# Optimization experiments

Measured on AMD Instinct MI355X. Metric: run time of the kernel, lower is better.

Reference implementation:

```python
import jax, jax.numpy as jnp
import numpy as np

V_PATCH = (1, 2, 4, 8, 16, 32)
SN = len(V_PATCH)
BETA = 0.25
RESI = 0.5  # abs(quant_resi)
K_PHI = 4
_ticks = np.linspace(1 / 3 / K_PHI, 1 - 1 / 3 / K_PHI, K_PHI)
PHI_SEL = [int(np.argmin(np.abs(_ticks - si / (SN - 1)))) for si in range(SN)]


def _bicubic_mat(n_in, n_out):
    # torch F.interpolate(mode='bicubic', align_corners=False): a=-0.75, half-pixel, edge clamp.
    a = -0.75
    M = np.zeros((n_out, n_in), np.float32)
    scale = n_in / n_out
    for i in range(n_out):
        x = (i + 0.5) * scale - 0.5
        x0 = int(np.floor(x))
        t = x - x0
        for j in range(-1, 3):
            d = abs(t - j)
            if d < 1.0:
                w = (a + 2) * d ** 3 - (a + 3) * d ** 2 + 1.0
            elif d < 2.0:
                w = a * d ** 3 - 5 * a * d ** 2 + 8 * a * d - 4 * a
            else:
                w = 0.0
            M[i, min(max(x0 + j, 0), n_in - 1)] += w
    return jnp.asarray(M)

_BICUBIC = {pn: _bicubic_mat(pn, V_PATCH[-1]) for pn in V_PATCH[:-1]}


def _phi(h, w, b):
    # Phi: h*(1-r) + Conv2d_3x3(h)*r
    y = jax.lax.conv_general_dilated(h, w, (1, 1), 'SAME',
                                     dimension_numbers=('NCHW', 'OIHW', 'NCHW'))
    y = y + b[None, :, None, None]
    return h * (1.0 - RESI) + y * RESI


def setup_inputs() -> dict:
    key = jax.random.key(0)
    k1, k2, k3, k4 = jax.random.split(key, 4)
    B, C, H = 32, 32, 32
    V = 4096
    return {
        'f_BChw': jax.random.normal(k1, (B, C, H, H), jnp.float32),
        'emb': jax.random.normal(k2, (V, C), jnp.float32) * 0.5,
        'phi_w': jax.random.normal(k3, (K_PHI, C, C, 3, 3), jnp.float32) * 0.05,
        'phi_b': jax.random.normal(k4, (K_PHI, C), jnp.float32) * 0.05,
    }


def reference(f_BChw, emb, phi_w, phi_b):
    f = f_BChw.astype(jnp.float32)
    B, C, H, W = f.shape
    V = emb.shape[0]
    f_ng = jax.lax.stop_gradient(f)
    f_rest = f_ng
    # NOTE: the original uses the NON-inplace `f_hat.add(h_BChw)` so f_hat never accumulates.
    f_hat = jnp.zeros_like(f)
    loss = jnp.float32(0.0)
    hits = jnp.zeros((V,), jnp.float32)
    e_sq = jnp.sum(emb * emb, axis=1)  # [V]
    for si, pn in enumerate(V_PATCH):
        if si != SN - 1:
            # mode='area' downsample; pn divides H so it is exact mean pooling
            r = f_rest.reshape(B, C, pn, H // pn, pn, W // pn).mean(axis=(3, 5))
        else:
            r = f_rest
        z = r.transpose(0, 2, 3, 1).reshape(-1, C)  # [N, C]
        d = jax.lax.stop_gradient(
            jnp.sum(z * z, axis=1, keepdims=True) + e_sq - 2.0 * (z @ emb.T))  # [N, V]
        idx = jnp.argmin(d, axis=1)
        hits = hits + jnp.bincount(idx, length=V).astype(jnp.float32)
        h = emb[idx].reshape(B, pn, pn, C).transpose(0, 3, 1, 2)  # [B, C, pn, pn]
        if si != SN - 1:
            M = _BICUBIC[pn]
            h = jnp.einsum('Hh,bchw,Ww->bcHW', M, h, M)
        h = _phi(h, phi_w[PHI_SEL[si]], phi_b[PHI_SEL[si]])
        # original: f_hat.add(h)  (result discarded -> no-op); f_rest.sub_(h) (in-place)
        f_rest = f_rest - h
        loss = loss + BETA * jnp.mean((jax.lax.stop_gradient(f_hat) - f) ** 2) \
                    + jnp.mean((f_hat - f_ng) ** 2)
    total = jnp.sum(hits)
    p = hits / jnp.maximum(total, 1.0)
    perplexity = jnp.exp(-jnp.sum(p * jnp.log(p + 1e-10)))
    return f_hat, loss, perplexity
```

## Files before the change

kernel.cpp:

```cpp
#include <hip/hip_runtime.h>
#include <math.h>
#include <float.h>

#define BS    32
#define CH    32
#define HH    32
#define VV    4096
#define FELEMS (BS*CH*HH*HH)
#define NROWS_TOTAL 43680

typedef unsigned short ushort_t;
typedef unsigned long long u64_t;
typedef _Float16 half_t;
typedef __attribute__((ext_vector_type(8))) _Float16 half8;
typedef __attribute__((ext_vector_type(4))) float floatx4;

__device__ inline void split2(float x, half_t* h, half_t* l) {
    half_t hh = (half_t)x;
    float r = x - (float)hh;
    *h = hh;
    *l = (half_t)r;
}

__device__ inline unsigned score_key32(float s) {
    unsigned u = __builtin_bit_cast(unsigned, s);
    unsigned m = (u & 0x80000000u) ? ~u : (u | 0x80000000u);
    return ~m;
}

__global__ __launch_bounds__(256) void prep_kernel(const float* __restrict__ f,
                                                   const float* __restrict__ emb,
                                                   const float* __restrict__ phw,
                                                   half_t* __restrict__ whi,
                                                   half_t* __restrict__ wlo,
                                                   half_t* __restrict__ ehi,
                                                   half_t* __restrict__ elo,
                                                   float* __restrict__ nesqh,
                                                   float* __restrict__ hits,
                                                   float* __restrict__ laccp,
                                                   half_t* __restrict__ zhi,
                                                   half_t* __restrict__ zlo,
                                                   u64_t* __restrict__ pk,
                                                   float* __restrict__ zpbase,
                                                   float* __restrict__ dout) {
    int gid = blockIdx.x * 256 + threadIdx.x;
    float4 z4 = {0.f, 0.f, 0.f, 0.f};
    *(float4*)(dout + (size_t)gid * 4) = z4;
    if (gid < VV) hits[gid] = 0.f;
    if (gid < NROWS_TOTAL) pk[gid] = ~0ull;
    for (int j = gid; j < 348160; j += 262144) zpbase[j] = 0.f;
    if (gid < 36864) {
        int k = gid & 7, c = (gid >> 3) & 15, q = (gid >> 7) & 3;
        int t2 = gid >> 9;
        int tau = t2 % 9, m2 = t2 / 9;
        int mt = m2 & 1, phi = m2 >> 1;
        int co = mt * 16 + c, ci = q * 8 + k;
        float w = phw[((size_t)(phi * 32 + co) * 32 + ci) * 9 + tau];
        half_t h, l; split2(w, &h, &l);
        whi[gid] = h; wlo[gid] = l;
    }
    if (gid < VV) {
        int v = gid;
        const float* ep = emb + (size_t)v * CH;
        float s = 0.f;
        half_t h[CH], l[CH];
#pragma unroll
        for (int i = 0; i < CH; i++) {
            float e = ep[i];
            s = fmaf(e, e, s);
            split2(e, &h[i], &l[i]);
        }
        nesqh[v] = -0.5f * s;
#pragma unroll
        for (int q = 0; q < 4; q++) {
            half8 H, L;
#pragma unroll
            for (int k = 0; k < 8; k++) {
                H[k] = h[q * 8 + k];
                L[k] = l[q * 8 + k];
            }
            *(half8*)(ehi + (size_t)v * CH + q * 8) = H;
            *(half8*)(elo + (size_t)v * CH + q * 8) = L;
        }
    }

    const int pair = blockIdx.x;
    const float* base = f + (size_t)pair * 1024;
    float s = 0.f, s2 = 0.f;
    for (int p = threadIdx.x; p < 1024; p += 256) {
        float v = base[p];
        s += v;
        s2 = fmaf(v, v, s2);
    }
    __shared__ float sh[256], sh2[256];
    sh[threadIdx.x] = s;
    sh2[threadIdx.x] = s2;
    __syncthreads();
    for (int o = 128; o > 0; o >>= 1) {
        if (threadIdx.x < o) {
            sh[threadIdx.x]  += sh[threadIdx.x + o];
            sh2[threadIdx.x] += sh2[threadIdx.x + o];
        }
        __syncthreads();
    }
    if (threadIdx.x == 0) {
        split2(sh[0] * (1.0f / 1024.0f), &zhi[pair], &zlo[pair]);
        laccp[pair] = sh2[0];
    }
}

__device__ inline floatx4 score_chain(half8 ah, half8 al,
                                      half8 bh, half8 bl, floatx4 ehv) {
    floatx4 acc;
    acc = __builtin_amdgcn_mfma_f32_16x16x32_f16(ah, bh, ehv, 0, 0, 0);
    acc = __builtin_amdgcn_mfma_f32_16x16x32_f16(ah, bl, acc, 0, 0, 0);
    acc = __builtin_amdgcn_mfma_f32_16x16x32_f16(al, bh, acc, 0, 0, 0);
    return acc;
}

__device__ inline void sel4(const floatx4& acc, int v, float* best, int* bidx) {
#pragma unroll
    for (int r = 0; r < 4; r++) {
        if (acc[r] > best[r]) { best[r] = acc[r]; bidx[r] = v; }
    }
}

template <int RT, int TPW>
__device__ inline void argmin_body(const half8* a1, const half8* a2,
                                   const half_t* __restrict__ ehi,
                                   const half_t* __restrict__ elo,
                                   const float* __restrict__ nesqh,
                                   u64_t* __restrict__ pk, int row0, int t0) {
    const int tid  = threadIdx.x;
    const int wv   = tid >> 6;
    const int lane = tid & 63;
    const int col  = lane & 15;
    const int quad = lane >> 4;

    float best[RT][4];
    int   bidx[RT][4];
#pragma unroll
    for (int rt = 0; rt < RT; rt++)
#pragma unroll
        for (int r = 0; r < 4; r++) { best[rt][r] = -FLT_MAX; bidx[rt][r] = 0; }

    int t = t0 + wv * TPW;
    const int tend = t + TPW;

    size_t eoff = ((size_t)((t << 4) + col) << 5) + (quad << 3);
    half8 nb1 = *(const half8*)(ehi + eoff);
    half8 nb2 = *(const half8*)(elo + eoff);
    float neh = nesqh[(t << 4) + col];

    floatx4 acc[RT];
    int vprev = 0;
    if (RT > 1) acc[RT - 1] = floatx4{-FLT_MAX, -FLT_MAX, -FLT_MAX, -FLT_MAX};

    for (; t < tend; t++) {
        const half8 b1 = nb1, b2 = nb2;
        const floatx4 ehv = {neh, neh, neh, neh};
        const int vcur = (t << 4) + col;
        const int tn = (t + 1 < tend) ? (t + 1) : t;
        const size_t eoff2 = ((size_t)((tn << 4) + col) << 5) + (quad << 3);
        nb1 = *(const half8*)(ehi + eoff2);
        nb2 = *(const half8*)(elo + eoff2);
        neh = nesqh[(tn << 4) + col];

        if (RT == 1) {
            acc[0] = score_chain(a1[0], a2[0], b1, b2, ehv);
            sel4(acc[0], vcur, best[0], bidx[0]);
        } else {
            acc[0] = score_chain(a1[0], a2[0], b1, b2, ehv);
            sel4(acc[RT - 1], vprev, best[RT - 1], bidx[RT - 1]);
#pragma unroll
            for (int rt = 1; rt < RT; rt++) {
                acc[rt] = score_chain(a1[rt], a2[rt], b1, b2, ehv);
                sel4(acc[rt - 1], vcur, best[rt - 1], bidx[rt - 1]);
            }
            vprev = vcur;
        }
    }
    if (RT > 1) sel4(acc[RT - 1], vprev, best[RT - 1], bidx[RT - 1]);

#pragma unroll
    for (int m = 1; m < 16; m <<= 1) {
#pragma unroll
        for (int rt = 0; rt < RT; rt++)
#pragma unroll
            for (int r = 0; r < 4; r++) {
                float s2 = __shfl_xor(best[rt][r], m, 64);
                int   v2 = __shfl_xor(bidx[rt][r], m, 64);
                if (s2 > best[rt][r] ||
                    (s2 == best[rt][r] && v2 < bidx[rt][r])) {
                    best[rt][r] = s2; bidx[rt][r] = v2;
                }
            }
    }

    __shared__ float sbs[4 * RT * 16];
    __shared__ int   sbi[4 * RT * 16];
    if (col == 0) {
#pragma unroll
        for (int rt = 0; rt < RT; rt++)
#pragma unroll
            for (int r = 0; r < 4; r++) {
                int row = rt * 16 + (quad << 2) + r;
                sbs[wv * RT * 16 + row] = best[rt][r];
                sbi[wv * RT * 16 + row] = bidx[rt][r];
            }
    }
    __syncthreads();
    if (tid < RT * 16) {
        float s = sbs[tid];
        int   v = sbi[tid];
        for (int w = 1; w < 4; w++) {
            float s2 = sbs[w * RT * 16 + tid];
            int   v2 = sbi[w * RT * 16 + tid];
            if (s2 > s || (s2 == s && v2 < v)) { s = s2; v = v2; }
        }
        u64_t key = ((u64_t)score_key32(s) << 32) | (unsigned)v;
        atomicMin(pk + row0 + tid, key);
    }
}

template <int RT, int VS>
__global__ __launch_bounds__(256) void argmin_stage(const half_t* __restrict__ zhi,
                                                    const half_t* __restrict__ zlo,
                                                    const half_t* __restrict__ ehi,
                                                    const half_t* __restrict__ elo,
                                                    const float* __restrict__ nesqh,
                                                    u64_t* __restrict__ pk) {
    const int lane = threadIdx.x & 63;
    const int col  = lane & 15;
    const int quad = lane >> 4;
    const int row0 = blockIdx.x * (16 * RT);

    half8 a1[RT], a2[RT];
#pragma unroll
    for (int rt = 0; rt < RT; rt++) {
        size_t off = ((size_t)(row0 + rt * 16 + col) << 5) + (quad << 3);
        a1[rt] = *(const half8*)(zhi + off);
        a2[rt] = *(const half8*)(zlo + off);
    }
    argmin_body<RT, 64 / VS>(a1, a2, ehi, elo, nesqh, pk,
                             row0, (int)blockIdx.y * (256 / VS));
}

template <int RT, int VS, int PN>
__global__ __launch_bounds__(256) void argmin_zp(const float* __restrict__ zp,
                                                 const half_t* __restrict__ ehi,
                                                 const half_t* __restrict__ elo,
                                                 const float* __restrict__ nesqh,
                                                 u64_t* __restrict__ pk) {
    const int lane = threadIdx.x & 63;
    const int col  = lane & 15;
    const int quad = lane >> 4;
    const int row0 = blockIdx.x * (16 * RT);
    constexpr int PSP = 32 / PN;
    const float scale = 1.0f / (float)(PSP * PSP);

    half8 a1[RT], a2[RT];
#pragma unroll
    for (int rt = 0; rt < RT; rt++) {
        const float* p = zp + (size_t)(row0 + rt * 16 + col) * CH + (quad << 3);
        float4 v0 = *(const float4*)p;
        float4 v1 = *(const float4*)(p + 4);
        float s[8] = {v0.x, v0.y, v0.z, v0.w, v1.x, v1.y, v1.z, v1.w};
#pragma unroll
        for (int k = 0; k < 8; k++) {
            half_t h, l;
            split2(s[k] * scale, &h, &l);
            a1[rt][k] = h; a2[rt][k] = l;
        }
    }
    argmin_body<RT, 64 / VS>(a1, a2, ehi, elo, nesqh, pk,
                             row0, (int)blockIdx.y * (256 / VS));
}

__global__ __launch_bounds__(256) void argmin5_fused(const float* __restrict__ frest,
                                                     const half_t* __restrict__ ehi,
                                                     const half_t* __restrict__ elo,
                                                     const float* __restrict__ nesqh,
                                                     u64_t* __restrict__ pk) {
    const int lane = threadIdx.x & 63;
    const int col  = lane & 15;
    const int quad = lane >> 4;
    const int row0 = blockIdx.x * 64;

    half8 a1[4], a2[4];
#pragma unroll
    for (int rt = 0; rt < 4; rt++) {
        int n = row0 + rt * 16 + col;
        int b = n >> 10, i = (n >> 5) & 31, j = n & 31;
        const float* p = frest + ((((size_t)(b * CH + quad * 8)) * HH + i) * HH + j);
#pragma unroll
        for (int k = 0; k < 8; k++) {
            half_t h, l;
            split2(p[(size_t)k * (HH * HH)], &h, &l);
            a1[rt][k] = h; a2[rt][k] = l;
        }
    }
    argmin_body<4, 32>(a1, a2, ehi, elo, nesqh, pk,
                       row0, (int)blockIdx.y * 128);
}

__device__ inline void cubic_w(float xs, int pn, int* ix, float* w) {
    const float a = -0.75f;
    float xf = floorf(xs);
    int x0 = (int)xf;
    float t = xs - xf;
#pragma unroll
    for (int j = -1; j <= 2; j++) {
        float d = fabsf(t - (float)j);
        float ww;
        if (d < 1.0f)      ww = ((a + 2.0f) * d - (a + 3.0f)) * d * d + 1.0f;
        else if (d < 2.0f) ww = ((a * d - 5.0f * a) * d + 8.0f * a) * d - 4.0f * a;
        else               ww = 0.0f;
        int xi = x0 + j;
        xi = xi < 0 ? 0 : (xi > pn - 1 ? pn - 1 : xi);
        ix[j + 1] = xi;
        w[j + 1]  = ww;
    }
}

template <int PN, int PN_NEXT>
__global__ __launch_bounds__(1024) void conv_mfma_kernel(const u64_t* __restrict__ pk,
                                                         const float* __restrict__ emb,
                                                         const half_t* __restrict__ whi,
                                                         const half_t* __restrict__ wlo,
                                                         const float* __restrict__ bias,
                                                         const float* __restrict__ src,
                                                         float* __restrict__ dst,
                                                         float* __restrict__ zp) {
    constexpr int IYB = (PN <= 4) ? PN : 6;
    const int t    = threadIdx.x;
    const int lane = t & 63, col = lane & 15, quad = lane >> 4;
    const int wid  = t >> 6;
    const int Nt   = wid >> 1, mt = wid & 1;
    const int ty   = Nt >> 1, xh = Nt & 1;
    const int yt   = blockIdx.x & 7, b = blockIdx.x >> 3;
    const int y0   = yt * 4;

    __shared__ half8 Hhi8[816], Hlo8[816];
    __shared__ float cache[IYB][PN][32];
    half_t* Hhi = (half_t*)Hhi8;
    half_t* Hlo = (half_t*)Hlo8;

    const float scale = (float)PN / (float)HH;
    int iy_lo = 0;
    if (PN > 4) {
        int lo = (int)floorf(((float)(y0 - 1) + 0.5f) * scale - 0.5f) - 1;
        lo = lo < 0 ? 0 : lo;
        lo = lo > PN - IYB ? PN - IYB : lo;
        iy_lo = lo;
    }

    const u64_t* pkb = pk + b * PN * PN;
    for (int i = t; i < IYB * PN * 8; i += 1024) {
        int chg = i & 7, cell = i >> 3;
        int ix = cell % PN, iyb = cell / PN;
        int idx = (int)(unsigned)(pkb[(iy_lo + iyb) * PN + ix] & 0xFFFFFFFFull);
        *(float4*)&cache[iyb][ix][chg * 4] =
            *(const float4*)(emb + (size_t)idx * CH + chg * 4);
    }
    __syncthreads();

    for (int i = t; i < 1632; i += 1024) {
        int chg = i & 7, cell = i >> 3;
        int xs = cell % 34, row = cell / 34;
        int gy = y0 - 1 + row, gx = xs - 1;
        float s0 = 0.f, s1 = 0.f, s2 = 0.f, s3 = 0.f;
        if ((unsigned)gy < 32u && (unsigned)gx < 32u) {
            int iy[4], ixv[4]; float wy[4], wxv[4];
            cubic_w(((float)gy + 0.5f) * scale - 0.5f, PN, iy, wy);
            cubic_w(((float)gx + 0.5f) * scale - 0.5f, PN, ixv, wxv);
#pragma unroll
            for (int a = 0; a < 4; a++) {
                const int iyb = iy[a] - iy_lo;
                float r0 = 0.f, r1 = 0.f, r2 = 0.f, r3 = 0.f;
#pragma unroll
                for (int b2 = 0; b2 < 4; b2++) {
                    const float4 tv = *(const float4*)&cache[iyb][ixv[b2]][chg * 4];
                    r0 = fmaf(tv.x, wxv[b2], r0);
                    r1 = fmaf(tv.y, wxv[b2], r1);
                    r2 = fmaf(tv.z, wxv[b2], r2);
                    r3 = fmaf(tv.w, wxv[b2], r3);
                }
                s0 = fmaf(r0, wy[a], s0);
                s1 = fmaf(r1, wy[a], s1);
                s2 = fmaf(r2, wy[a], s2);
                s3 = fmaf(r3, wy[a], s3);
            }
        }
        const int ho = cell * 32 + chg * 4;
        half_t h, l;
        split2(s0, &h, &l); Hhi[ho + 0] = h; Hlo[ho + 0] = l;
        split2(s1, &h, &l); Hhi[ho + 1] = h; Hlo[ho + 1] = l;
        split2(s2, &h, &l); Hhi[ho + 2] = h; Hlo[ho + 2] = l;
        split2(s3, &h, &l); Hhi[ho + 3] = h; Hlo[ho + 3] = l;
    }
    __syncthreads();

    const float4 bv = *(const float4*)(bias + mt * 16 + quad * 4);
    floatx4 acc = {bv.x, bv.y, bv.z, bv.w};
#pragma unroll
    for (int tau = 0; tau < 9; tau++) {
        const int dy = tau / 3, dx = tau % 3;
        const int woff = (mt * 9 + tau) * 512 + quad * 128 + col * 8;
        const half8 wh = *(const half8*)(whi + woff);
        const half8 wl = *(const half8*)(wlo + woff);
        const int hoff = ((ty + dy) * 34 + xh * 16 + dx + col) * 32 + quad * 8;
        const half8 hh = *(const half8*)(Hhi + hoff);
        const half8 hl = *(const half8*)(Hlo + hoff);
        acc = __builtin_amdgcn_mfma_f32_16x16x32_f16(wh, hh, acc, 0, 0, 0);
        acc = __builtin_amdgcn_mfma_f32_16x16x32_f16(wh, hl, acc, 0, 0, 0);
        acc = __builtin_amdgcn_mfma_f32_16x16x32_f16(wl, hh, acc, 0, 0, 0);
    }

    const int x = xh * 16 + col, y = y0 + ty;
    const int hcell = ((ty + 1) * 34 + (x + 1)) * 32;
    float pv[4];
#pragma unroll
    for (int r = 0; r < 4; r++) {
        const int c = mt * 16 + quad * 4 + r;
        const float hc = (float)Hhi[hcell + c] + (float)Hlo[hcell + c];
        const size_t off = (((size_t)(b * CH + c)) * HH + y) * HH + x;
        const float dv = src[off] - (0.5f * hc + 0.5f * acc[r]);
        dst[off] = dv;
        pv[r] = dv;
    }

    if constexpr (PN_NEXT != 0) {
        constexpr int PSP = 32 / PN_NEXT;
#pragma unroll
        for (int m = 1; m < PSP; m <<= 1)
#pragma unroll
            for (int r = 0; r < 4; r++) pv[r] += __shfl_xor(pv[r], m, 64);
        if ((col & (PSP - 1)) == 0) {
            const int wx = x / PSP, wy = y / PSP;
#pragma unroll
            for (int r = 0; r < 4; r++) {
                const int c = mt * 16 + quad * 4 + r;
                atomicAdd(zp + ((size_t)((b * PN_NEXT + wy) * PN_NEXT + wx)) * CH + c,
                          pv[r]);
            }
        }
    }
}

__global__ __launch_bounds__(256) void bincount_kernel(const u64_t* __restrict__ pk,
                                                       float* __restrict__ hits, int n) {
    int i = blockIdx.x * 256 + threadIdx.x;
    if (i < n) {
        int idx = (int)(unsigned)(pk[i] & 0xFFFFFFFFull);
        atomicAdd(&hits[idx], 1.0f);
    }
}

__global__ __launch_bounds__(256) void finalize_kernel(const float* __restrict__ hits,
                                                       const float* __restrict__ laccp,
                                                       float* __restrict__ outs) {
    __shared__ float sh[256];
    int t = threadIdx.x;
    const float tot = (float)NROWS_TOTAL;
    float ent = 0.f;
    for (int v = t; v < VV; v += 256) {
        float p = hits[v] / tot;
        ent += p * logf(p + 1e-10f);
    }
    sh[t] = ent;
    __syncthreads();
    for (int o = 128; o > 0; o >>= 1) {
        if (t < o) sh[t] += sh[t + o];
        __syncthreads();
    }
    float entT = sh[0];
    __syncthreads();
    float ls = 0.f;
    for (int i = t; i < 1024; i += 256) ls += laccp[i];
    sh[t] = ls;
    __syncthreads();
    for (int o = 128; o > 0; o >>= 1) {
        if (t < o) sh[t] += sh[t + o];
        __syncthreads();
    }
    if (t == 0) {
        outs[0] = 7.5f * sh[0] * (1.0f / (float)FELEMS);
        outs[1] = expf(-entT);
    }
}

extern "C" void kernel_launch(void* const* d_in, const int* in_sizes, int n_in,
                              void* d_out, int out_size, void* d_ws, size_t ws_size,
                              hipStream_t stream) {
    const float* f   = (const float*)d_in[0];
    const float* emb = (const float*)d_in[1];
    const float* phw = (const float*)d_in[2];
    const float* phb = (const float*)d_in[3];
    float* out = (float*)d_out;

    float* ws      = (float*)d_ws;
    float* hits    = ws;
    float* laccp   = ws + 4096;
    u64_t* pkbase  = (u64_t*)(ws + 8448);
    float* frest   = ws + 95808;
    half_t* zhi    = (half_t*)(ws + 1144384);
    half_t* zlo    = (half_t*)(ws + 1275456);
    float* nesqh   = ws + 1537600;
    half_t* ehi    = (half_t*)(ws + 2590272);
    half_t* elo    = (half_t*)(ws + 2655808);
    float* zp      = ws + 2721344;
    half_t* whi    = (half_t*)(ws + 3069504);
    half_t* wlo    = (half_t*)(ws + 3087936);

    float* zp1 = zp;
    float* zp2 = zp + 4096;
    float* zp3 = zp + 20480;
    float* zp4 = zp + 86016;

    prep_kernel<<<1024, 256, 0, stream>>>(f, emb, phw, whi, wlo, ehi, elo, nesqh,
                                          hits, laccp, zhi, zlo, pkbase, zp, out);

    const int pkoff[6] = {0, 32, 160, 672, 2720, 10912};
    const size_t WFP = 9216;

    argmin_stage<1, 16><<<dim3(2, 16), 256, 0, stream>>>(zhi, zlo, ehi, elo, nesqh,
                                                         pkbase + pkoff[0]);
    conv_mfma_kernel<1, 2><<<256, 1024, 0, stream>>>(pkbase + pkoff[0], emb,
                                                     whi + 0 * WFP, wlo + 0 * WFP,
                                                     phb + 0 * CH, f, frest, zp1);

    argmin_zp<1, 16, 2><<<dim3(8, 16), 256, 0, stream>>>(zp1, ehi, elo, nesqh,
                                                         pkbase + pkoff[1]);
    conv_mfma_kernel<2, 4><<<256, 1024, 0, stream>>>(pkbase + pkoff[1], emb,
                                                     whi + 0 * WFP, wlo + 0 * WFP,
                                                     phb + 0 * CH, frest, frest, zp2);

    argmin_zp<1, 16, 4><<<dim3(32, 16), 256, 0, stream>>>(zp2, ehi, elo, nesqh,
                                                          pkbase + pkoff[2]);
    conv_mfma_kernel<4, 8><<<256, 1024, 0, stream>>>(pkbase + pkoff[2], emb,
                                                     whi + 1 * WFP, wlo + 1 * WFP,
                                                     phb + 1 * CH, frest, frest, zp3);

    argmin_zp<1, 8, 8><<<dim3(128, 8), 256, 0, stream>>>(zp3, ehi, elo, nesqh,
                                                         pkbase + pkoff[3]);
    conv_mfma_kernel<8, 16><<<256, 1024, 0, stream>>>(pkbase + pkoff[3], emb,
                                                      whi + 2 * WFP, wlo + 2 * WFP,
                                                      phb + 2 * CH, frest, frest, zp4);

    argmin_zp<2, 4, 16><<<dim3(256, 4), 256, 0, stream>>>(zp4, ehi, elo, nesqh,
                                                          pkbase + pkoff[4]);
    conv_mfma_kernel<16, 0><<<256, 1024, 0, stream>>>(pkbase + pkoff[4], emb,
                                                      whi + 3 * WFP, wlo + 3 * WFP,
                                                      phb + 3 * CH, frest, frest, nullptr);

    argmin5_fused<<<dim3(512, 2), 256, 0, stream>>>(frest, ehi, elo, nesqh,
                                                    pkbase + pkoff[5]);

    bincount_kernel<<<(NROWS_TOTAL + 255) / 256, 256, 0, stream>>>(pkbase, hits, NROWS_TOTAL);
    finalize_kernel<<<1, 256, 0, stream>>>(hits, laccp, out + (out_size - 2));
}
```

Measured before the change: 202.8 us.

## Split argmin work by rows across waves instead of codebook slices for big stages

For the two largest argmin stages (16x16 and 32x32), each wave now owns its own set of query rows and scans a shared codebook slice, instead of all four waves sharing rows and splitting the codebook. This removes the cross-wave shared-memory reduction, so each block writes four times as many rows directly through atomicMin. The grid also has more codebook slices along y. The aim is to give each block more independent rows per codebook fetch and a cheaper reduction. The cost is more atomics on the packed keys and different codebook reuse across waves.

```diff
diff --git a/kernel.cpp b/kernel.cpp
--- a/kernel.cpp
+++ b/kernel.cpp
@@ -126,6 +126,75 @@
 }
 
 template <int RT, int TPW>
+__device__ inline void argmin_scan(const half8* a1, const half8* a2,
+                                   const half_t* __restrict__ ehi,
+                                   const half_t* __restrict__ elo,
+                                   const float* __restrict__ nesqh,
+                                   int t0, float best[RT][4], int bidx[RT][4]) {
+    const int lane = threadIdx.x & 63;
+    const int col  = lane & 15;
+    const int quad = lane >> 4;
+
+#pragma unroll
+    for (int rt = 0; rt < RT; rt++)
+#pragma unroll
+        for (int r = 0; r < 4; r++) { best[rt][r] = -FLT_MAX; bidx[rt][r] = 0; }
+
+    int t = t0;
+    const int tend = t0 + TPW;
+
+    size_t eoff = ((size_t)((t << 4) + col) << 5) + (quad << 3);
+    half8 nb1 = *(const half8*)(ehi + eoff);
+    half8 nb2 = *(const half8*)(elo + eoff);
+    float neh = nesqh[(t << 4) + col];
+
+    floatx4 acc[RT];
+    int vprev = 0;
+    if (RT > 1) acc[RT - 1] = floatx4{-FLT_MAX, -FLT_MAX, -FLT_MAX, -FLT_MAX};
+
+    for (; t < tend; t++) {
+        const half8 b1 = nb1, b2 = nb2;
+        const floatx4 ehv = {neh, neh, neh, neh};
+        const int vcur = (t << 4) + col;
+        const int tn = (t + 1 < tend) ? (t + 1) : t;
+        const size_t eoff2 = ((size_t)((tn << 4) + col) << 5) + (quad << 3);
+        nb1 = *(const half8*)(ehi + eoff2);
+        nb2 = *(const half8*)(elo + eoff2);
+        neh = nesqh[(tn << 4) + col];
+
+        if (RT == 1) {
+            acc[0] = score_chain(a1[0], a2[0], b1, b2, ehv);
+            sel4(acc[0], vcur, best[0], bidx[0]);
+        } else {
+            acc[0] = score_chain(a1[0], a2[0], b1, b2, ehv);
+            sel4(acc[RT - 1], vprev, best[RT - 1], bidx[RT - 1]);
+#pragma unroll
+            for (int rt = 1; rt < RT; rt++) {
+                acc[rt] = score_chain(a1[rt], a2[rt], b1, b2, ehv);
+                sel4(acc[rt - 1], vcur, best[rt - 1], bidx[rt - 1]);
+            }
+            vprev = vcur;
+        }
+    }
+    if (RT > 1) sel4(acc[RT - 1], vprev, best[RT - 1], bidx[RT - 1]);
+
+#pragma unroll
+    for (int m = 1; m < 16; m <<= 1) {
+#pragma unroll
+        for (int rt = 0; rt < RT; rt++)
+#pragma unroll
+            for (int r = 0; r < 4; r++) {
+                float s2 = __shfl_xor(best[rt][r], m, 64);
+                int   v2 = __shfl_xor(bidx[rt][r], m, 64);
+                if (s2 > best[rt][r] ||
+                    (s2 == best[rt][r] && v2 < bidx[rt][r])) {
+                    best[rt][r] = s2; bidx[rt][r] = v2;
+                }
+            }
+    }
+}
+
+template <int RT, int TPW>
 __device__ inline void argmin_body(const half8* a1, const half8* a2,
                                    const half_t* __restrict__ ehi,
                                    const half_t* __restrict__ elo,
@@ -139,63 +208,7 @@
 
     float best[RT][4];
     int   bidx[RT][4];
-#pragma unroll
-    for (int rt = 0; rt < RT; rt++)
-#pragma unroll
-        for (int r = 0; r < 4; r++) { best[rt][r] = -FLT_MAX; bidx[rt][r] = 0; }
-
-    int t = t0 + wv * TPW;
-    const int tend = t + TPW;
-
-    size_t eoff = ((size_t)((t << 4) + col) << 5) + (quad << 3);
-    half8 nb1 = *(const half8*)(ehi + eoff);
-    half8 nb2 = *(const half8*)(elo + eoff);
-    float neh = nesqh[(t << 4) + col];
-
-    floatx4 acc[RT];
-    int vprev = 0;
-    if (RT > 1) acc[RT - 1] = floatx4{-FLT_MAX, -FLT_MAX, -FLT_MAX, -FLT_MAX};
-
-    for (; t < tend; t++) {
-        const half8 b1 = nb1, b2 = nb2;
-        const floatx4 ehv = {neh, neh, neh, neh};
-        const int vcur = (t << 4) + col;
-        const int tn = (t + 1 < tend) ? (t + 1) : t;
-        const size_t eoff2 = ((size_t)((tn << 4) + col) << 5) + (quad << 3);
-        nb1 = *(const half8*)(ehi + eoff2);
-        nb2 = *(const half8*)(elo + eoff2);
-        neh = nesqh[(tn << 4) + col];
-
-        if (RT == 1) {
-            acc[0] = score_chain(a1[0], a2[0], b1, b2, ehv);
-            sel4(acc[0], vcur, best[0], bidx[0]);
-        } else {
-            acc[0] = score_chain(a1[0], a2[0], b1, b2, ehv);
-            sel4(acc[RT - 1], vprev, best[RT - 1], bidx[RT - 1]);
-#pragma unroll
-            for (int rt = 1; rt < RT; rt++) {
-                acc[rt] = score_chain(a1[rt], a2[rt], b1, b2, ehv);
-                sel4(acc[rt - 1], vcur, best[rt - 1], bidx[rt - 1]);
-            }
-            vprev = vcur;
-        }
-    }
-    if (RT > 1) sel4(acc[RT - 1], vprev, best[RT - 1], bidx[RT - 1]);
-
-#pragma unroll
-    for (int m = 1; m < 16; m <<= 1) {
-#pragma unroll
-        for (int rt = 0; rt < RT; rt++)
-#pragma unroll
-            for (int r = 0; r < 4; r++) {
-                float s2 = __shfl_xor(best[rt][r], m, 64);
-                int   v2 = __shfl_xor(bidx[rt][r], m, 64);
-                if (s2 > best[rt][r] ||
-                    (s2 == best[rt][r] && v2 < bidx[rt][r])) {
-                    best[rt][r] = s2; bidx[rt][r] = v2;
-                }
-            }
-    }
+    argmin_scan<RT, TPW>(a1, a2, ehi, elo, nesqh, t0 + wv * TPW, best, bidx);
 
     __shared__ float sbs[4 * RT * 16];
     __shared__ int   sbi[4 * RT * 16];
@@ -220,6 +233,41 @@
         }
         u64_t key = ((u64_t)score_key32(s) << 32) | (unsigned)v;
         atomicMin(pk + row0 + tid, key);
+    }
+}
+
+template <int RT, int TPW>
+__device__ inline void argmin_body_rs(const half8* a1, const half8* a2,
+                                      const half_t* __restrict__ ehi,
+                                      const half_t* __restrict__ elo,
+                                      const float* __restrict__ nesqh,
+                                      u64_t* __restrict__ pk, int blockRow0, int t0) {
+    const int tid  = threadIdx.x;
+    const int wv   = tid >> 6;
+    const int lane = tid & 63;
+    const int col  = lane & 15;
+    const int quad = lane >> 4;
+
+    float best[RT][4];
+    int   bidx[RT][4];
+    argmin_scan<RT, TPW>(a1, a2, ehi, elo, nesqh, t0, best, bidx);
+
+    __shared__ float sbs[4 * RT * 16];
+    __shared__ int   sbi[4 * RT * 16];
+    if (col == 0) {
+#pragma unroll
+        for (int rt = 0; rt < RT; rt++)
+#pragma unroll
+            for (int r = 0; r < 4; r++) {
+                int row = rt * 16 + (quad << 2) + r;
+                sbs[wv * RT * 16 + row] = best[rt][r];
+                sbi[wv * RT * 16 + row] = bidx[rt][r];
+            }
+    }
+    __syncthreads();
+    if (tid < 4 * RT * 16) {
+        u64_t key = ((u64_t)score_key32(sbs[tid]) << 32) | (unsigned)sbi[tid];
+        atomicMin(pk + blockRow0 + tid, key);
     }
 }
 
@@ -277,20 +325,55 @@
                              row0, (int)blockIdx.y * (256 / VS));
 }
 
-__global__ __launch_bounds__(256) void argmin5_fused(const float* __restrict__ frest,
-                                                     const half_t* __restrict__ ehi,
-                                                     const half_t* __restrict__ elo,
-                                                     const float* __restrict__ nesqh,
-                                                     u64_t* __restrict__ pk) {
+template <int RT, int VS, int PN>
+__global__ __launch_bounds__(256) void argmin_zp_rs(const float* __restrict__ zp,
+                                                    const half_t* __restrict__ ehi,
+                                                    const half_t* __restrict__ elo,
+                                                    const float* __restrict__ nesqh,
+                                                    u64_t* __restrict__ pk) {
     const int lane = threadIdx.x & 63;
     const int col  = lane & 15;
     const int quad = lane >> 4;
-    const int row0 = blockIdx.x * 64;
+    const int wv   = threadIdx.x >> 6;
+    const int blockRow0 = blockIdx.x * (64 * RT);
+    const int row0w = blockRow0 + wv * (16 * RT);
+    constexpr int PSP = 32 / PN;
+    const float scale = 1.0f / (float)(PSP * PSP);
+
+    half8 a1[RT], a2[RT];
+#pragma unroll
+    for (int rt = 0; rt < RT; rt++) {
+        const float* p = zp + (size_t)(row0w + rt * 16 + col) * CH + (quad << 3);
+        float4 v0 = *(const float4*)p;
+        float4 v1 = *(const float4*)(p + 4);
+        float s[8] = {v0.x, v0.y, v0.z, v0.w, v1.x, v1.y, v1.z, v1.w};
+#pragma unroll
+        for (int k = 0; k < 8; k++) {
+            half_t h, l;
+            split2(s[k] * scale, &h, &l);
+            a1[rt][k] = h; a2[rt][k] = l;
+        }
+    }
+    argmin_body_rs<RT, 256 / VS>(a1, a2, ehi, elo, nesqh, pk,
+                                 blockRow0, (int)blockIdx.y * (256 / VS));
+}
+
+__global__ __launch_bounds__(256) void argmin5_rs(const float* __restrict__ frest,
+                                                  const half_t* __restrict__ ehi,
+                                                  const half_t* __restrict__ elo,
+                                                  const float* __restrict__ nesqh,
+                                                  u64_t* __restrict__ pk) {
+    const int lane = threadIdx.x & 63;
+    const int col  = lane & 15;
+    const int quad = lane >> 4;
+    const int wv   = threadIdx.x >> 6;
+    const int blockRow0 = blockIdx.x * 256;
+    const int row0w = blockRow0 + wv * 64;
 
     half8 a1[4], a2[4];
 #pragma unroll
     for (int rt = 0; rt < 4; rt++) {
-        int n = row0 + rt * 16 + col;
+        int n = row0w + rt * 16 + col;
         int b = n >> 10, i = (n >> 5) & 31, j = n & 31;
         const float* p = frest + ((((size_t)(b * CH + quad * 8)) * HH + i) * HH + j);
 #pragma unroll
@@ -300,8 +383,8 @@
             a1[rt][k] = h; a2[rt][k] = l;
         }
     }
-    argmin_body<4, 32>(a1, a2, ehi, elo, nesqh, pk,
-                       row0, (int)blockIdx.y * 128);
+    argmin_body_rs<4, 32>(a1, a2, ehi, elo, nesqh, pk,
+                          blockRow0, (int)blockIdx.y * 32);
 }
 
 __device__ inline void cubic_w(float xs, int pn, int* ix, float* w) {
@@ -548,14 +631,14 @@
                                                       whi + 2 * WFP, wlo + 2 * WFP,
                                                       phb + 2 * CH, frest, frest, zp4);
 
-    argmin_zp<2, 4, 16><<<dim3(256, 4), 256, 0, stream>>>(zp4, ehi, elo, nesqh,
-                                                          pkbase + pkoff[4]);
+    argmin_zp_rs<2, 16, 16><<<dim3(64, 16), 256, 0, stream>>>(zp4, ehi, elo, nesqh,
+                                                              pkbase + pkoff[4]);
     conv_mfma_kernel<16, 0><<<256, 1024, 0, stream>>>(pkbase + pkoff[4], emb,
                                                       whi + 3 * WFP, wlo + 3 * WFP,
                                                       phb + 3 * CH, frest, frest, nullptr);
 
-    argmin5_fused<<<dim3(512, 2), 256, 0, stream>>>(frest, ehi, elo, nesqh,
-                                                    pkbase + pkoff[5]);
+    argmin5_rs<<<dim3(128, 8), 256, 0, stream>>>(frest, ehi, elo, nesqh,
+                                                 pkbase + pkoff[5]);
 
     bincount_kernel<<<(NROWS_TOTAL + 255) / 256, 256, 0, stream>>>(pkbase, hits, NROWS_TOTAL);
     finalize_kernel<<<1, 256, 0, stream>>>(hits, laccp, out + (out_size - 2));
```

Result: slower. 233.3 us (+15.1%).
